# Kernel optimization log

Measured on AMD Instinct MI355X. Metric: run time of the kernel, lower is better.

The kernel has to match this reference:

```python
import jax, jax.numpy as jnp
import numpy as np
from jax import lax

B, T, C, H, W = 1, 6, 64, 128, 128
DG, K = 16, 9          # deformable groups, 3x3 kernel positions
CG = C // DG
MRM = 10.0             # max_residue_magnitude


def _conv3(x, w, b):
    y = lax.conv_general_dilated(x, w, (1, 1), 'SAME',
                                 dimension_numbers=('NCHW', 'OIHW', 'NCHW'))
    return y + b[None, :, None, None]


def _leaky(x):
    return jnp.where(x >= 0, x, 0.1 * x)


def _bilinear(img, py, px):
    # img [N,Cc,h,w]; py/px [N,*S] unnormalized pixel coords; zero padding outside.
    N, Cc, h, w = img.shape
    S = py.shape[1:]
    py = py.reshape(N, -1)
    px = px.reshape(N, -1)
    y0 = jnp.floor(py); x0 = jnp.floor(px)
    fy = py - y0; fx = px - x0
    y0 = y0.astype(jnp.int32); x0 = x0.astype(jnp.int32)
    imf = img.reshape(N, Cc, h * w)

    def corner(yi, xi, wt):
        valid = (yi >= 0) & (yi < h) & (xi >= 0) & (xi < w)
        idx = jnp.clip(yi, 0, h - 1) * w + jnp.clip(xi, 0, w - 1)
        v = jax.vmap(lambda im, ix: im[:, ix])(imf, idx)  # [N,Cc,M]
        return v * (wt * valid)[:, None, :]

    out = (corner(y0, x0, (1 - fy) * (1 - fx))
           + corner(y0, x0 + 1, (1 - fy) * fx)
           + corner(y0 + 1, x0, fy * (1 - fx))
           + corner(y0 + 1, x0 + 1, fy * fx))
    return out.reshape(N, Cc, *S)


def _flow_warp(x, flow):
    # flow [N,2,H,W]: channel 0 = x-displacement, channel 1 = y-displacement
    gy = jnp.arange(H, dtype=jnp.float32)
    gx = jnp.arange(W, dtype=jnp.float32)
    py = gy[None, :, None] + flow[:, 1]
    px = gx[None, None, :] + flow[:, 0]
    return _bilinear(x, py, px)


def _mod_deform_conv(x, offset, mask, w, b):
    # offset [N, 2*DG*K, H, W] interleaved (y,x) per (group, kernel pos); mask [N, DG*K, H, W]
    N = x.shape[0]
    off = offset.reshape(N, DG, K, 2, H, W)
    kh = (jnp.arange(K) // 3).astype(jnp.float32)
    kw = (jnp.arange(K) % 3).astype(jnp.float32)
    gy = jnp.arange(H, dtype=jnp.float32)
    gx = jnp.arange(W, dtype=jnp.float32)
    # stride 1, padding 1, dilation 1, 3x3 kernel
    py = gy[None, None, None, :, None] - 1.0 + kh[None, None, :, None, None] + off[:, :, :, 0]
    px = gx[None, None, None, None, :] - 1.0 + kw[None, None, :, None, None] + off[:, :, :, 1]
    xg = x.reshape(N, DG, CG, H, W).reshape(N * DG, CG, H, W)
    s = _bilinear(xg, py.reshape(N * DG, K, H, W), px.reshape(N * DG, K, H, W))
    s = s.reshape(N, DG, CG, K, H, W) * mask.reshape(N, DG, 1, K, H, W)
    wr = w.reshape(C, DG, CG, K)
    return jnp.einsum('ngckhw,ogck->nohw', s, wr) + b[None, :, None, None]


def setup_inputs() -> dict:
    key = jax.random.key(0)
    ks = jax.random.split(key, 10)
    rn = lambda k, s, sc: jax.random.normal(k, s, jnp.float32) * sc
    cin = 2 * C + 2  # (1 + n_frames//2)*C + n_frames
    return {
        'x': rn(ks[0], (B, T, C, H, W), 1.0),
        'flows_backward': rn(ks[1], (B, T - 1, 2, H, W), 2.0),
        'flows_forward': rn(ks[2], (B, T - 1, 2, H, W), 2.0),
        'cw1': rn(ks[3], (C, cin, 3, 3), 1.0 / np.sqrt(cin * 9)),
        'cb1': jnp.zeros((C,), jnp.float32),
        'cw2': rn(ks[4], (C, C, 3, 3), 1.0 / np.sqrt(C * 9)),
        'cb2': jnp.zeros((C,), jnp.float32),
        'cw3': rn(ks[5], (C, C, 3, 3), 1.0 / np.sqrt(C * 9)),
        'cb3': jnp.zeros((C,), jnp.float32),
        # original zero-inits the last conv; use small random so offsets/masks are nontrivial
        'cw4': rn(ks[6], (3 * K * DG, C, 3, 3), 0.01),
        'cb4': jnp.zeros((3 * K * DG,), jnp.float32),
        'dcn_w': rn(ks[7], (C, C, 3, 3), 1.0 / np.sqrt(C * 9)),
        'dcn_b': jnp.zeros((C,), jnp.float32),
    }


def reference(x, flows_backward, flows_forward, cw1, cb1, cw2, cb2, cw3, cb3,
              cw4, cb4, dcn_w, dcn_b):
    # Batch all backward-pass frame pairs (i=T-1..1) and forward-pass pairs (i=0..T-2)
    # into one effective batch of B*2*(T-1) independent DCN calls.
    xi = jnp.concatenate([x[:, 1:], x[:, :-1]], axis=1)      # source frames
    cur = jnp.concatenate([x[:, :-1], x[:, 1:]], axis=1)     # target (current) frames
    fl = jnp.concatenate([flows_backward, flows_forward], axis=1)
    N = B * 2 * (T - 1)
    xi = xi.reshape(N, C, H, W)
    cur = cur.reshape(N, C, H, W)
    fl = fl.reshape(N, 2, H, W)

    warped = _flow_warp(xi, fl)
    inp = jnp.concatenate([warped, cur, fl], axis=1)          # [N, 2C+2, H, W]
    h1 = _leaky(_conv3(inp, cw1, cb1))
    h2 = _leaky(_conv3(h1, cw2, cb2))
    h3 = _leaky(_conv3(h2, cw3, cb3))
    out = _conv3(h3, cw4, cb4)                                # [N, 3*9*DG, H, W]
    o1, o2, m = jnp.split(out, 3, axis=1)
    offset = MRM * jnp.tanh(jnp.concatenate([o1, o2], axis=1))
    # flow.flip(1).repeat -> interleaved (fy, fx) added to every (group, kernel pos)
    offset = offset + jnp.tile(fl[:, ::-1], (1, DG * K, 1, 1))
    mask = jax.nn.sigmoid(m)

    feat = _mod_deform_conv(xi, offset, mask, dcn_w, dcn_b)   # [N, C, H, W]
    feat = feat.reshape(B, 2, T - 1, C, H, W)
    zeros = jnp.zeros((B, 1, C, H, W), feat.dtype)
    x_backward = jnp.concatenate([feat[:, 0], zeros], axis=1)  # [B, T, C, H, W]
    x_forward = jnp.concatenate([zeros, feat[:, 1]], axis=1)   # [B, T, C, H, W]
    return x_backward, x_forward
```

## Files before the change

kernel.cpp:

```cpp
#include <hip/hip_runtime.h>
#include <math.h>

#define NP   10
#define C_   64
#define H_   128
#define W_   128
#define HW   (H_*W_)
#define MRM_ 10.0f

#define A_OFF   0u
#define SV_OFF  41472u
#define OMB_OFF 66048u
#define LDS_TOT 81408

#define W1T_N 82944
#define W2T_N 36864
#define W4_N  294912
#define DWT_N 49152

typedef __bf16 bf16x8 __attribute__((ext_vector_type(8)));
typedef float  f32x16 __attribute__((ext_vector_type(16)));

__device__ __forceinline__ f32x16 mfma32(bf16x8 a, bf16x8 b, f32x16 c) {
    return __builtin_amdgcn_mfma_f32_32x32x16_bf16(a, b, c, 0, 0, 0);
}

__device__ __forceinline__ ushort bfrn(float f) {
    uint u = __builtin_bit_cast(uint, f);
    u += 0x7FFFu + ((u >> 16) & 1u);
    return (ushort)(u >> 16);
}
__device__ __forceinline__ float blo(uint u) { return __builtin_bit_cast(float, u << 16); }
__device__ __forceinline__ float bhi(uint u) { return __builtin_bit_cast(float, u & 0xFFFF0000u); }
__device__ __forceinline__ float fast_tanh(float x) {
    float e = __expf(2.f * x);
    return 1.f - 2.f / (e + 1.f);
}

__device__ __forceinline__ const float* xi_base(const float* x, int n) {
    int f = (n < 5) ? (n + 1) : (n - 5);
    return x + (size_t)f * C_ * HW;
}
__device__ __forceinline__ const float* cur_base(const float* x, int n) {
    int f = (n < 5) ? n : (n - 4);
    return x + (size_t)f * C_ * HW;
}
__device__ __forceinline__ const float* fl_base(const float* fb, const float* ff, int n) {
    return (n < 5) ? (fb + (size_t)n * 2 * HW) : (ff + (size_t)(n - 5) * 2 * HW);
}

struct Bil { int i00, i01, i10, i11; float m00, m01, m10, m11; };
__device__ __forceinline__ Bil bil(float py, float px) {
    float y0f = floorf(py), x0f = floorf(px);
    int iy0 = (int)y0f, ix0 = (int)x0f;
    float ay = py - y0f, ax = px - x0f;
    bool v0y = (unsigned)iy0 < (unsigned)H_;
    bool v1y = (unsigned)(iy0 + 1) < (unsigned)H_;
    bool v0x = (unsigned)ix0 < (unsigned)W_;
    bool v1x = (unsigned)(ix0 + 1) < (unsigned)W_;
    int cy0 = min(max(iy0, 0), H_ - 1), cy1 = min(max(iy0 + 1, 0), H_ - 1);
    int cx0 = min(max(ix0, 0), W_ - 1), cx1 = min(max(ix0 + 1, 0), W_ - 1);
    Bil r;
    r.m00 = (1.f - ay) * (1.f - ax) * (float)(v0y && v0x);
    r.m01 = (1.f - ay) * ax         * (float)(v0y && v1x);
    r.m10 = ay * (1.f - ax)         * (float)(v1y && v0x);
    r.m11 = ay * ax                 * (float)(v1y && v1x);
    r.i00 = cy0 * W_ + cx0; r.i01 = cy0 * W_ + cx1;
    r.i10 = cy1 * W_ + cx0; r.i11 = cy1 * W_ + cx1;
    return r;
}

__global__ __launch_bounds__(256) void k_prep(
        const float* __restrict__ cw1, const float* __restrict__ cw2,
        const float* __restrict__ cw3, const float* __restrict__ cw4,
        const float* __restrict__ cb4, const float* __restrict__ dw,
        ushort* __restrict__ w1t, ushort* __restrict__ w2t,
        ushort* __restrict__ w3t, ushort* __restrict__ w4t,
        ushort* __restrict__ dwtb, float* __restrict__ pb4) {
    int id = blockIdx.x * 256 + threadIdx.x;
    if (id < W1T_N) {
        int blk = id >> 9, e = id & 511;
        int c = blk / 18, r = blk % 18; int t = r >> 1, nf = r & 1;
        int l = e >> 3, j = e & 7;
        int ci = c * 16 + (l >> 5) * 8 + j;
        int oc = nf * 32 + (l & 31);
        w1t[id] = (ci < 130) ? bfrn(cw1[((size_t)oc * 130 + ci) * 9 + t]) : (ushort)0;
        return;
    }
    id -= W1T_N;
    if (id < W2T_N) {
        int blk = id >> 9, e = id & 511;
        int c = blk / 18, r = blk % 18; int t = r >> 1, nf = r & 1;
        int l = e >> 3, j = e & 7;
        int ci = c * 16 + (l >> 5) * 8 + j;
        int oc = nf * 32 + (l & 31);
        w2t[id] = bfrn(cw2[((size_t)oc * 64 + ci) * 9 + t]);
        return;
    }
    id -= W2T_N;
    if (id < W2T_N) {
        int blk = id >> 9, e = id & 511;
        int c = blk / 18, r = blk % 18; int t = r >> 1, nf = r & 1;
        int l = e >> 3, j = e & 7;
        int ci = c * 16 + (l >> 5) * 8 + j;
        int oc = nf * 32 + (l & 31);
        w3t[id] = bfrn(cw3[((size_t)oc * 64 + ci) * 9 + t]);
        return;
    }
    id -= W2T_N;
    if (id < W4_N) {
        int blk = id >> 9, e = id & 511;
        int c = blk / 144, r = blk - c * 144;
        int t = r >> 4, g = r & 15;
        int l = e >> 3, j = e & 7;
        int nn = l & 31, kh = l >> 5;
        int ci = c * 16 + kh * 8 + j;
        int ch = (nn < 18) ? g * 18 + nn : (nn < 27 ? 288 + g * 9 + (nn - 18) : -1);
        float v = (ch >= 0) ? cw4[((size_t)ch * 64 + ci) * 9 + t] : 0.f;
        w4t[id] = bfrn(v);
        return;
    }
    id -= W4_N;
    if (id < DWT_N) {
        int blk = id >> 9, e = id & 511;
        int g = blk / 6, r = blk - g * 6;
        int kst = r >> 1, nf = r & 1;
        int l = e >> 3, j = e & 7;
        int kk = kst * 16 + (l >> 5) * 8 + j;
        int oc = nf * 32 + (l & 31);
        float v = (kk < 36) ? dw[((size_t)oc * 64 + g * 4 + (kk & 3)) * 9 + (kk >> 2)] : 0.f;
        dwtb[id] = bfrn(v);
        return;
    }
    id -= DWT_N;
    if (id < 512) {
        int g = id >> 5, nn = id & 31;
        int ch = (nn < 18) ? g * 18 + nn : (nn < 27 ? 288 + g * 9 + (nn - 18) : -1);
        pb4[id] = (ch >= 0) ? cb4[ch] : 0.f;
    }
}

__global__ __launch_bounds__(256) void k_warp(
        const float* __restrict__ x, const float* __restrict__ fb,
        const float* __restrict__ ff, ushort* __restrict__ warped) {
    int gid = blockIdx.x * 256 + threadIdx.x;
    int n = gid / HW, pos = gid % HW;
    int y = pos / W_, xx = pos % W_;
    const float* fl = fl_base(fb, ff, n);
    float fx = fl[pos], fy = fl[HW + pos];
    Bil b = bil((float)y + fy, (float)xx + fx);
    const float* xb = xi_base(x, n);
    ushort* wout = warped + (size_t)n * C_ * HW + pos;
    for (int c = 0; c < C_; ++c) {
        const float* p = xb + c * HW;
        wout[c * HW] = bfrn(b.m00 * p[b.i00] + b.m01 * p[b.i01]
                          + b.m10 * p[b.i10] + b.m11 * p[b.i11]);
    }
}

__global__ __launch_bounds__(256) void k_xt(
        const float* __restrict__ x, ushort* __restrict__ xt) {
    int gid = blockIdx.x * 256 + threadIdx.x;
    int f = gid / HW, pos = gid % HW;
    const float* src = x + (size_t)f * C_ * HW + pos;
    ushort* dst = xt + (size_t)f * 16 * HW * 4;
    #pragma unroll
    for (int g = 0; g < 16; ++g) {
        uint2 v;
        ushort h0 = bfrn(src[(g * 4 + 0) * HW]);
        ushort h1 = bfrn(src[(g * 4 + 1) * HW]);
        ushort h2 = bfrn(src[(g * 4 + 2) * HW]);
        ushort h3 = bfrn(src[(g * 4 + 3) * HW]);
        v.x = (uint)h0 | ((uint)h1 << 16);
        v.y = (uint)h2 | ((uint)h3 << 16);
        *(uint2*)(dst + ((size_t)g * HW + pos) * 4) = v;
    }
}

template<int NCHUNK, int SRC>
__global__ __launch_bounds__(256, 3) void k_convm(
        const ushort* __restrict__ inb, const float* __restrict__ x,
        const float* __restrict__ fb, const float* __restrict__ ff,
        const ushort* __restrict__ wt, const float* __restrict__ bias,
        ushort* __restrict__ outp) {
    __shared__ __align__(16) char ldsb[41472];
    int tid = threadIdx.x;
    int lane = tid & 63, w = tid >> 6;
    int id = (blockIdx.x & 7) * 80 + (blockIdx.x >> 3);
    int bx = id & 7, by = (id >> 3) & 7, n = id >> 6;
    int col = lane & 31, khalf = lane >> 5;

    const float* flp = fl_base(fb, ff, n);
    const float* curp = cur_base(x, n);

    f32x16 acc[2][2];
    #pragma unroll
    for (int a = 0; a < 2; ++a)
        #pragma unroll
        for (int b = 0; b < 2; ++b)
            #pragma unroll
            for (int r = 0; r < 16; ++r) acc[a][b][r] = 0.f;

    int xb2 = col & 15;
    int rb0 = 4 * w + ((col >> 4) & 1);
    const int NPASS = (NCHUNK + 3) / 4;

    #pragma unroll
    for (int p = 0; p < NPASS; ++p) {
        const int c0 = 4 * p;
        const int cN = (NCHUNK - c0 >= 4) ? 4 : (NCHUNK - c0);
        __syncthreads();
        for (int cc = 0; cc < cN; ++cc) {
            int chunk = c0 + cc;
            int cbase = chunk * 16 + w * 4;
            for (int v = 0; v < 6; ++v) {
                int cell = v * 64 + lane;
                if (cell < 324) {
                    int cy = cell / 18, cx = cell - cy * 18;
                    int gy = by * 16 + cy - 1, gx = bx * 16 + cx - 1;
                    bool ok = ((unsigned)gy < 128u) && ((unsigned)gx < 128u);
                    int pos = gy * W_ + gx;
                    uint2 hv; hv.x = hv.y = 0;
                    if (SRC == 1 || chunk < 4) {
                        const ushort* sp = inb + ((size_t)n * 64 + cbase) * HW + pos;
                        ushort h0 = ok ? sp[0] : (ushort)0;
                        ushort h1 = ok ? sp[HW] : (ushort)0;
                        ushort h2 = ok ? sp[2 * HW] : (ushort)0;
                        ushort h3 = ok ? sp[3 * HW] : (ushort)0;
                        hv.x = (uint)h0 | ((uint)h1 << 16);
                        hv.y = (uint)h2 | ((uint)h3 << 16);
                    } else if (chunk < 8) {
                        const float* sp = curp + (size_t)(cbase - 64) * HW + pos;
                        ushort h0 = bfrn(ok ? sp[0] : 0.f);
                        ushort h1 = bfrn(ok ? sp[HW] : 0.f);
                        ushort h2 = bfrn(ok ? sp[2 * HW] : 0.f);
                        ushort h3 = bfrn(ok ? sp[3 * HW] : 0.f);
                        hv.x = (uint)h0 | ((uint)h1 << 16);
                        hv.y = (uint)h2 | ((uint)h3 << 16);
                    } else {
                        float v0 = 0.f, v1 = 0.f;
                        if (w == 0 && ok) { v0 = flp[pos]; v1 = flp[HW + pos]; }
                        hv.x = (uint)bfrn(v0) | ((uint)bfrn(v1) << 16);
                    }
                    uint byte = (uint)cell * 128 + (uint)cc * 32 + (uint)w * 8;
                    byte ^= ((uint)(cell & 7)) << 4;
                    *(uint2*)(ldsb + byte) = hv;
                }
            }
        }
        __syncthreads();
        for (int cc = 0; cc < cN; ++cc) {
            #pragma unroll
            for (int t = 0; t < 9; ++t) {
                const int ky = t / 3, kx = t % 3;
                size_t bb = (size_t)(((c0 + cc) * 9 + t) * 2) * 512 + (size_t)lane * 8;
                bf16x8 b0 = *(const bf16x8*)(wt + bb);
                bf16x8 b1 = *(const bf16x8*)(wt + bb + 512);
                #pragma unroll
                for (int f = 0; f < 2; ++f) {
                    int cell = (rb0 + 2 * f + ky) * 18 + xb2 + kx;
                    uint byte = (uint)cell * 128 + (uint)(2 * cc + khalf) * 16;
                    byte ^= ((uint)(cell & 7)) << 4;
                    bf16x8 a = *(const bf16x8*)(ldsb + byte);
                    acc[f][0] = mfma32(a, b0, acc[f][0]);
                    acc[f][1] = mfma32(a, b1, acc[f][1]);
                }
            }
        }
    }

    ushort* op = outp + (size_t)n * 64 * HW;
    #pragma unroll
    for (int f = 0; f < 2; ++f)
        #pragma unroll
        for (int nf = 0; nf < 2; ++nf) {
            int oc = nf * 32 + col;
            float bs = bias[oc];
            #pragma unroll
            for (int r = 0; r < 16; ++r) {
                int pxl = 64 * w + 32 * f + (r & 3) + 8 * (r >> 2) + 4 * khalf;
                int y = by * 16 + (pxl >> 4), xx = bx * 16 + (pxl & 15);
                float v = acc[f][nf][r] + bs;
                v = (v >= 0.f) ? v : 0.1f * v;
                op[(size_t)oc * HW + y * W_ + xx] = bfrn(v);
            }
        }
}

__global__ __launch_bounds__(256, 2) void k_dcn7(
        const ushort* __restrict__ h3, const ushort* __restrict__ xt,
        const float* __restrict__ fb, const float* __restrict__ ff,
        const ushort* __restrict__ w4hi,
        const ushort* __restrict__ dwtb, const float* __restrict__ pb4,
        const float* __restrict__ db, float* __restrict__ outb) {
    extern __shared__ __align__(16) char lds[];
    _Float16* OMBH = (_Float16*)(lds + OMB_OFF);

    int tid = threadIdx.x;
    int lane = tid & 63, w = tid >> 6;
    int id = (blockIdx.x & 7) * 80 + (blockIdx.x >> 3);
    int bx = id & 7, by = (id >> 3) & 7, n = id >> 6;
    int col = lane & 31, khalf = lane >> 5;

    const ushort* h3n = h3 + (size_t)n * 64 * HW;
    const float* fl = fl_base(fb, ff, n);
    int fxi = (n < 5) ? (n + 1) : (n - 5);
    const ushort* xtn = xt + (size_t)fxi * 16 * HW * 4;

    int Yp = by * 16 + (tid >> 4), Xp = bx * 16 + (tid & 15);
    float fxr = fl[Yp * W_ + Xp];
    float fyr = fl[HW + Yp * W_ + Xp];

    {
        uint pb = SV_OFF + (uint)tid * 96 + 72;
        *(unsigned long long*)(lds + pb)      = 0ull;
        *(unsigned long long*)(lds + pb + 8)  = 0ull;
        *(unsigned long long*)(lds + pb + 16) = 0ull;
    }

    for (int c = 0; c < 4; ++c) {
        for (int v = 0; v < 6; ++v) {
            int cell = v * 64 + lane;
            if (cell < 324) {
                int cy = cell / 18, cx = cell - cy * 18;
                int gy = by * 16 + cy - 1, gx = bx * 16 + cx - 1;
                bool ok = ((unsigned)gy < 128u) && ((unsigned)gx < 128u);
                const ushort* srcp = h3n + (size_t)(c * 16 + w * 4) * HW + gy * W_ + gx;
                ushort h0 = ok ? srcp[0] : (ushort)0;
                ushort h1 = ok ? srcp[HW] : (ushort)0;
                ushort h2 = ok ? srcp[2 * HW] : (ushort)0;
                ushort h3v = ok ? srcp[3 * HW] : (ushort)0;
                uint2 hv;
                hv.x = (uint)h0 | ((uint)h1 << 16);
                hv.y = (uint)h2 | ((uint)h3v << 16);
                uint byte = (uint)cell * 128 + (uint)c * 32 + (uint)w * 8;
                byte ^= ((uint)(cell & 7)) << 4;
                *(uint2*)(lds + byte) = hv;
            }
        }
    }
    __syncthreads();

    f32x16 zero16;
    #pragma unroll
    for (int r = 0; r < 16; ++r) zero16[r] = 0.f;

    f32x16 cd[2][2];
    #pragma unroll
    for (int a = 0; a < 2; ++a)
        #pragma unroll
        for (int b = 0; b < 2; ++b) cd[a][b] = zero16;

    int xb2 = col & 15;
    int rb0 = 4 * w + ((col >> 4) & 1);

    for (int sp = 0; sp < 8; ++sp) {
        int g0 = sp * 2;
        f32x16 c4[2][2];
        #pragma unroll
        for (int a = 0; a < 2; ++a)
            #pragma unroll
            for (int b = 0; b < 2; ++b) c4[a][b] = zero16;

        #pragma unroll 1
        for (int c = 0; c < 4; ++c) {
            #pragma unroll
            for (int t = 0; t < 9; ++t) {
                const int ky = t / 3, kx = t % 3;
                size_t bb = (size_t)((c * 9 + t) * 16) * 512 + (size_t)lane * 8;
                bf16x8 bh0 = *(const bf16x8*)(w4hi + bb + (size_t)g0 * 512);
                bf16x8 bh1 = *(const bf16x8*)(w4hi + bb + (size_t)(g0 + 1) * 512);
                #pragma unroll
                for (int f = 0; f < 2; ++f) {
                    int cell = (rb0 + 2 * f + ky) * 18 + xb2 + kx;
                    uint byte = (uint)cell * 128 + (uint)(2 * c + khalf) * 16;
                    byte ^= ((uint)(cell & 7)) << 4;
                    bf16x8 ah = *(const bf16x8*)(lds + byte);
                    c4[0][f] = mfma32(ah, bh0, c4[0][f]);
                    c4[1][f] = mfma32(ah, bh1, c4[1][f]);
                }
            }
        }

        #pragma unroll
        for (int gg = 0; gg < 2; ++gg) {
            int g = g0 + gg;
            __builtin_amdgcn_sched_barrier(0);
            if (col < 27) {
                float pb = pb4[g * 32 + col];
                #pragma unroll
                for (int f = 0; f < 2; ++f)
                    #pragma unroll
                    for (int r = 0; r < 16; ++r) {
                        int pxl = 64 * w + 32 * f + (r & 3) + 8 * (r >> 2) + 4 * khalf;
                        float v = c4[gg][f][r] + pb;
                        v = (col < 18) ? MRM_ * fast_tanh(v) : 1.f / (1.f + __expf(-v));
                        OMBH[pxl * 30 + col] = (_Float16)v;
                    }
            }
            __builtin_amdgcn_sched_barrier(0);
            {
                int px = tid;
                float Yf = (float)Yp, Xf = (float)Xp;
                const ushort* xg = xtn + (size_t)g * HW * 4;
                #pragma unroll
                for (int k = 0; k < 9; ++k) {
                    float oy = (float)OMBH[px * 30 + 2 * k] + fyr;
                    float ox = (float)OMBH[px * 30 + 2 * k + 1] + fxr;
                    float mk = (float)OMBH[px * 30 + 18 + k];
                    Bil b = bil(Yf - 1.f + (float)(k / 3) + oy,
                                Xf - 1.f + (float)(k % 3) + ox);
                    uint2 q00 = *(const uint2*)(xg + (size_t)b.i00 * 4);
                    uint2 q01 = *(const uint2*)(xg + (size_t)b.i01 * 4);
                    uint2 q10 = *(const uint2*)(xg + (size_t)b.i10 * 4);
                    uint2 q11 = *(const uint2*)(xg + (size_t)b.i11 * 4);
                    float s0 = b.m00 * blo(q00.x) + b.m01 * blo(q01.x)
                             + b.m10 * blo(q10.x) + b.m11 * blo(q11.x);
                    float s1 = b.m00 * bhi(q00.x) + b.m01 * bhi(q01.x)
                             + b.m10 * bhi(q10.x) + b.m11 * bhi(q11.x);
                    float s2 = b.m00 * blo(q00.y) + b.m01 * blo(q01.y)
                             + b.m10 * blo(q10.y) + b.m11 * blo(q11.y);
                    float s3 = b.m00 * bhi(q00.y) + b.m01 * bhi(q01.y)
                             + b.m10 * bhi(q10.y) + b.m11 * bhi(q11.y);
                    uint2 pk;
                    pk.x = (uint)bfrn(s0 * mk) | ((uint)bfrn(s1 * mk) << 16);
                    pk.y = (uint)bfrn(s2 * mk) | ((uint)bfrn(s3 * mk) << 16);
                    *(uint2*)(lds + (SV_OFF + (uint)px * 96 + (uint)k * 8)) = pk;
                }
            }
            __builtin_amdgcn_sched_barrier(0);
            #pragma unroll
            for (int kst = 0; kst < 3; ++kst) {
                size_t dbb = (size_t)((g * 3 + kst) * 2) * 512 + (size_t)lane * 8;
                bf16x8 b0 = *(const bf16x8*)(dwtb + dbb);
                bf16x8 b1 = *(const bf16x8*)(dwtb + dbb + 512);
                #pragma unroll
                for (int f = 0; f < 2; ++f) {
                    int pxl = 64 * w + 32 * f + col;
                    uint byte = SV_OFF + (uint)pxl * 96 + (uint)(kst * 2 + khalf) * 16;
                    bf16x8 a = *(const bf16x8*)(lds + byte);
                    cd[f][0] = mfma32(a, b0, cd[f][0]);
                    cd[f][1] = mfma32(a, b1, cd[f][1]);
                }
            }
        }
    }

    float* base = (n < 5) ? outb + (size_t)n * 64 * HW
                          : outb + (size_t)(n + 2) * 64 * HW;
    #pragma unroll
    for (int f = 0; f < 2; ++f)
        #pragma unroll
        for (int nf = 0; nf < 2; ++nf) {
            int oc = nf * 32 + col;
            float bias = db[oc];
            #pragma unroll
            for (int r = 0; r < 16; ++r) {
                int pxl = 64 * w + 32 * f + (r & 3) + 8 * (r >> 2) + 4 * khalf;
                int y = by * 16 + (pxl >> 4), xx = bx * 16 + (pxl & 15);
                base[(size_t)oc * HW + y * W_ + xx] = cd[f][nf][r] + bias;
            }
        }
}

extern "C" void kernel_launch(void* const* d_in, const int* in_sizes, int n_in,
                              void* d_out, int out_size, void* d_ws, size_t ws_size,
                              hipStream_t stream) {
    (void)in_sizes; (void)n_in; (void)out_size; (void)ws_size;
    const float* x   = (const float*)d_in[0];
    const float* fb  = (const float*)d_in[1];
    const float* ff  = (const float*)d_in[2];
    const float* cw1 = (const float*)d_in[3];
    const float* cb1 = (const float*)d_in[4];
    const float* cw2 = (const float*)d_in[5];
    const float* cb2 = (const float*)d_in[6];
    const float* cw3 = (const float*)d_in[7];
    const float* cb3 = (const float*)d_in[8];
    const float* cw4 = (const float*)d_in[9];
    const float* cb4 = (const float*)d_in[10];
    const float* dw  = (const float*)d_in[11];
    const float* db  = (const float*)d_in[12];
    float* out = (float*)d_out;

    ushort* h1b  = (ushort*)d_ws;
    ushort* h3b  = h1b + 10485760;
    ushort* w1t  = h3b + 10485760;
    ushort* w2t  = w1t + W1T_N;
    ushort* w3t  = w2t + W2T_N;
    ushort* w4t  = w3t + W2T_N;
    ushort* dwtb = w4t + W4_N;
    float*  pb4  = (float*)(dwtb + DWT_N);
    ushort* xtb  = h1b;
    ushort* wpb  = (ushort*)d_out;
    ushort* h2b  = wpb + 10485760;

    (void)hipFuncSetAttribute((const void*)k_dcn7,
                              hipFuncAttributeMaxDynamicSharedMemorySize, LDS_TOT);

    k_prep<<<1958, 256, 0, stream>>>(cw1, cw2, cw3, cw4, cb4, dw,
                                     w1t, w2t, w3t, w4t, dwtb, pb4);
    k_warp<<<(NP * HW) / 256, 256, 0, stream>>>(x, fb, ff, wpb);
    k_convm<9, 0><<<640, 256, 0, stream>>>(wpb, x, fb, ff, w1t, cb1, h1b);
    k_convm<4, 1><<<640, 256, 0, stream>>>(h1b, x, fb, ff, w2t, cb2, h2b);
    k_xt<<<(6 * HW) / 256, 256, 0, stream>>>(x, xtb);
    k_convm<4, 1><<<640, 256, 0, stream>>>(h2b, x, fb, ff, w3t, cb3, h3b);

    hipMemsetAsync((char*)d_out + (size_t)5 * C_ * HW * sizeof(float), 0, (size_t)C_ * HW * sizeof(float), stream);
    hipMemsetAsync((char*)d_out + (size_t)6 * C_ * HW * sizeof(float), 0, (size_t)C_ * HW * sizeof(float), stream);

    k_dcn7<<<640, 256, LDS_TOT, stream>>>(h3b, xtb, fb, ff, w4t, dwtb, pb4, db, out);
}
```

Measured before the change: 618.1 us.

## Shrink DCN tile to 16x8 and pass sampled values via ds_bpermute

Splits the fused offset-conv and deformable-conv kernel into 128-thread blocks covering 16x8 pixel tiles, doubling the grid and shrinking the LDS footprint so more blocks can be resident. Bilinearly sampled, mask-weighted values now stay in registers and are routed to the MFMA A-operand layout with ds_bpermute instead of a round trip through an LDS staging buffer. The cost is a larger halo overhead relative to tile size when loading h3, more cross-lane permute instructions, and more blocks re-reading the same weights.

```diff
diff --git a/kernel.cpp b/kernel.cpp
--- a/kernel.cpp
+++ b/kernel.cpp
@@ -8,10 +8,8 @@
 #define HW   (H_*W_)
 #define MRM_ 10.0f
 
-#define A_OFF   0u
-#define SV_OFF  41472u
-#define OMB_OFF 66048u
-#define LDS_TOT 81408
+#define OMB8_OFF 23040u
+#define LDS8_TOT 30720
 
 #define W1T_N 82944
 #define W2T_N 36864
@@ -287,19 +285,19 @@
         }
 }
 
-__global__ __launch_bounds__(256, 2) void k_dcn7(
+__global__ __launch_bounds__(128, 2) void k_dcn8(
         const ushort* __restrict__ h3, const ushort* __restrict__ xt,
         const float* __restrict__ fb, const float* __restrict__ ff,
         const ushort* __restrict__ w4hi,
         const ushort* __restrict__ dwtb, const float* __restrict__ pb4,
         const float* __restrict__ db, float* __restrict__ outb) {
-    extern __shared__ __align__(16) char lds[];
-    _Float16* OMBH = (_Float16*)(lds + OMB_OFF);
+    __shared__ __align__(16) char lds[LDS8_TOT];
+    _Float16* OMBH = (_Float16*)(lds + OMB8_OFF);
 
     int tid = threadIdx.x;
     int lane = tid & 63, w = tid >> 6;
-    int id = (blockIdx.x & 7) * 80 + (blockIdx.x >> 3);
-    int bx = id & 7, by = (id >> 3) & 7, n = id >> 6;
+    int id = (blockIdx.x & 7) * 160 + (blockIdx.x >> 3);
+    int bx = id & 15, by = (id >> 4) & 7, n = id >> 7;
     int col = lane & 31, khalf = lane >> 5;
 
     const ushort* h3n = h3 + (size_t)n * 64 * HW;
@@ -307,35 +305,35 @@
     int fxi = (n < 5) ? (n + 1) : (n - 5);
     const ushort* xtn = xt + (size_t)fxi * 16 * HW * 4;
 
-    int Yp = by * 16 + (tid >> 4), Xp = bx * 16 + (tid & 15);
+    int Yp = by * 16 + (tid >> 3), Xp = bx * 8 + (tid & 7);
     float fxr = fl[Yp * W_ + Xp];
     float fyr = fl[HW + Yp * W_ + Xp];
 
-    {
-        uint pb = SV_OFF + (uint)tid * 96 + 72;
-        *(unsigned long long*)(lds + pb)      = 0ull;
-        *(unsigned long long*)(lds + pb + 8)  = 0ull;
-        *(unsigned long long*)(lds + pb + 16) = 0ull;
-    }
-
     for (int c = 0; c < 4; ++c) {
-        for (int v = 0; v < 6; ++v) {
+        for (int v = 0; v < 3; ++v) {
             int cell = v * 64 + lane;
-            if (cell < 324) {
-                int cy = cell / 18, cx = cell - cy * 18;
-                int gy = by * 16 + cy - 1, gx = bx * 16 + cx - 1;
+            if (cell < 180) {
+                int cy = cell / 10, cx = cell - cy * 10;
+                int gy = by * 16 + cy - 1, gx = bx * 8 + cx - 1;
                 bool ok = ((unsigned)gy < 128u) && ((unsigned)gx < 128u);
-                const ushort* srcp = h3n + (size_t)(c * 16 + w * 4) * HW + gy * W_ + gx;
-                ushort h0 = ok ? srcp[0] : (ushort)0;
-                ushort h1 = ok ? srcp[HW] : (ushort)0;
-                ushort h2 = ok ? srcp[2 * HW] : (ushort)0;
-                ushort h3v = ok ? srcp[3 * HW] : (ushort)0;
-                uint2 hv;
-                hv.x = (uint)h0 | ((uint)h1 << 16);
-                hv.y = (uint)h2 | ((uint)h3v << 16);
-                uint byte = (uint)cell * 128 + (uint)c * 32 + (uint)w * 8;
+                const ushort* srcp = h3n + (size_t)(c * 16 + w * 8) * HW + gy * W_ + gx;
+                uint2 hv0, hv1;
+                ushort q0 = ok ? srcp[0] : (ushort)0;
+                ushort q1 = ok ? srcp[HW] : (ushort)0;
+                ushort q2 = ok ? srcp[2 * HW] : (ushort)0;
+                ushort q3 = ok ? srcp[3 * HW] : (ushort)0;
+                ushort q4 = ok ? srcp[4 * HW] : (ushort)0;
+                ushort q5 = ok ? srcp[5 * HW] : (ushort)0;
+                ushort q6 = ok ? srcp[6 * HW] : (ushort)0;
+                ushort q7 = ok ? srcp[7 * HW] : (ushort)0;
+                hv0.x = (uint)q0 | ((uint)q1 << 16);
+                hv0.y = (uint)q2 | ((uint)q3 << 16);
+                hv1.x = (uint)q4 | ((uint)q5 << 16);
+                hv1.y = (uint)q6 | ((uint)q7 << 16);
+                uint byte = (uint)cell * 128 + (uint)c * 32 + (uint)w * 16;
                 byte ^= ((uint)(cell & 7)) << 4;
-                *(uint2*)(lds + byte) = hv;
+                *(uint2*)(lds + byte) = hv0;
+                *(uint2*)(lds + byte + 8) = hv1;
             }
         }
     }
@@ -351,8 +349,9 @@
         #pragma unroll
         for (int b = 0; b < 2; ++b) cd[a][b] = zero16;
 
-    int xb2 = col & 15;
-    int rb0 = 4 * w + ((col >> 4) & 1);
+    int colq = col >> 3;
+    int colx = col & 7;
+    int ad0 = (lane & 31) * 4;
 
     for (int sp = 0; sp < 8; ++sp) {
         int g0 = sp * 2;
@@ -372,7 +371,7 @@
                 bf16x8 bh1 = *(const bf16x8*)(w4hi + bb + (size_t)(g0 + 1) * 512);
                 #pragma unroll
                 for (int f = 0; f < 2; ++f) {
-                    int cell = (rb0 + 2 * f + ky) * 18 + xb2 + kx;
+                    int cell = (8 * w + 4 * f + colq + ky) * 10 + colx + kx;
                     uint byte = (uint)cell * 128 + (uint)(2 * c + khalf) * 16;
                     byte ^= ((uint)(cell & 7)) << 4;
                     bf16x8 ah = *(const bf16x8*)(lds + byte);
@@ -399,6 +398,7 @@
                     }
             }
             __builtin_amdgcn_sched_barrier(0);
+            int pkx[9], pky[9];
             {
                 int px = tid;
                 float Yf = (float)Yp, Xf = (float)Xp;
@@ -422,13 +422,10 @@
                              + b.m10 * blo(q10.y) + b.m11 * blo(q11.y);
                     float s3 = b.m00 * bhi(q00.y) + b.m01 * bhi(q01.y)
                              + b.m10 * bhi(q10.y) + b.m11 * bhi(q11.y);
-                    uint2 pk;
-                    pk.x = (uint)bfrn(s0 * mk) | ((uint)bfrn(s1 * mk) << 16);
-                    pk.y = (uint)bfrn(s2 * mk) | ((uint)bfrn(s3 * mk) << 16);
-                    *(uint2*)(lds + (SV_OFF + (uint)px * 96 + (uint)k * 8)) = pk;
+                    pkx[k] = (int)((uint)bfrn(s0 * mk) | ((uint)bfrn(s1 * mk) << 16));
+                    pky[k] = (int)((uint)bfrn(s2 * mk) | ((uint)bfrn(s3 * mk) << 16));
                 }
             }
-            __builtin_amdgcn_sched_barrier(0);
             #pragma unroll
             for (int kst = 0; kst < 3; ++kst) {
                 size_t dbb = (size_t)((g * 3 + kst) * 2) * 512 + (size_t)lane * 8;
@@ -436,9 +433,31 @@
                 bf16x8 b1 = *(const bf16x8*)(dwtb + dbb + 512);
                 #pragma unroll
                 for (int f = 0; f < 2; ++f) {
-                    int pxl = 64 * w + 32 * f + col;
-                    uint byte = SV_OFF + (uint)pxl * 96 + (uint)(kst * 2 + khalf) * 16;
-                    bf16x8 a = *(const bf16x8*)(lds + byte);
+                    int ad = ad0 + f * 128;
+                    uint a0, a1, a2, a3;
+                    if (kst < 2) {
+                        const int t0 = kst * 4;
+                        uint x0 = (uint)__builtin_amdgcn_ds_bpermute(ad, pkx[t0]);
+                        uint y0 = (uint)__builtin_amdgcn_ds_bpermute(ad, pky[t0]);
+                        uint x1 = (uint)__builtin_amdgcn_ds_bpermute(ad, pkx[t0 + 1]);
+                        uint y1 = (uint)__builtin_amdgcn_ds_bpermute(ad, pky[t0 + 1]);
+                        uint x2 = (uint)__builtin_amdgcn_ds_bpermute(ad, pkx[t0 + 2]);
+                        uint y2 = (uint)__builtin_amdgcn_ds_bpermute(ad, pky[t0 + 2]);
+                        uint x3 = (uint)__builtin_amdgcn_ds_bpermute(ad, pkx[t0 + 3]);
+                        uint y3 = (uint)__builtin_amdgcn_ds_bpermute(ad, pky[t0 + 3]);
+                        a0 = khalf ? x2 : x0;
+                        a1 = khalf ? y2 : y0;
+                        a2 = khalf ? x3 : x1;
+                        a3 = khalf ? y3 : y1;
+                    } else {
+                        uint x8 = (uint)__builtin_amdgcn_ds_bpermute(ad, pkx[8]);
+                        uint y8 = (uint)__builtin_amdgcn_ds_bpermute(ad, pky[8]);
+                        a0 = khalf ? 0u : x8;
+                        a1 = khalf ? 0u : y8;
+                        a2 = 0u; a3 = 0u;
+                    }
+                    uint4 av; av.x = a0; av.y = a1; av.z = a2; av.w = a3;
+                    bf16x8 a = __builtin_bit_cast(bf16x8, av);
                     cd[f][0] = mfma32(a, b0, cd[f][0]);
                     cd[f][1] = mfma32(a, b1, cd[f][1]);
                 }
@@ -457,7 +476,7 @@
             #pragma unroll
             for (int r = 0; r < 16; ++r) {
                 int pxl = 64 * w + 32 * f + (r & 3) + 8 * (r >> 2) + 4 * khalf;
-                int y = by * 16 + (pxl >> 4), xx = bx * 16 + (pxl & 15);
+                int y = by * 16 + (pxl >> 3), xx = bx * 8 + (pxl & 7);
                 base[(size_t)oc * HW + y * W_ + xx] = cd[f][nf][r] + bias;
             }
         }
@@ -494,9 +513,6 @@
     ushort* wpb  = (ushort*)d_out;
     ushort* h2b  = wpb + 10485760;
 
-    (void)hipFuncSetAttribute((const void*)k_dcn7,
-                              hipFuncAttributeMaxDynamicSharedMemorySize, LDS_TOT);
-
     k_prep<<<1958, 256, 0, stream>>>(cw1, cw2, cw3, cw4, cb4, dw,
                                      w1t, w2t, w3t, w4t, dwtb, pb4);
     k_warp<<<(NP * HW) / 256, 256, 0, stream>>>(x, fb, ff, wpb);
@@ -508,5 +524,5 @@
     hipMemsetAsync((char*)d_out + (size_t)5 * C_ * HW * sizeof(float), 0, (size_t)C_ * HW * sizeof(float), stream);
     hipMemsetAsync((char*)d_out + (size_t)6 * C_ * HW * sizeof(float), 0, (size_t)C_ * HW * sizeof(float), stream);
 
-    k_dcn7<<<640, 256, LDS_TOT, stream>>>(h3b, xtb, fb, ff, w4t, dwtb, pb4, db, out);
-}
+    k_dcn8<<<1280, 128, 0, stream>>>(h3b, xtb, fb, ff, w4t, dwtb, pb4, db, out);
+}
```

New measurement: 597.4 us. -3.3%, faster.
